# Kernel tuning notes

Measured on AMD Instinct MI355X. Metric: run time of the kernel, lower is better.

The kernel has to match this reference:

```python
import jax, jax.numpy as jnp
import numpy as np

B, T, C, H = 2, 2048, 1024, 16
D = C // H  # head dim = 64

def setup_inputs() -> dict:
    key = jax.random.key(0)
    ks = jax.random.split(key, 6)
    s = 0.02
    return {
        "x":  jax.random.normal(ks[0], (B, T, C), dtype=jnp.float32),
        "Wk": jax.random.normal(ks[1], (C, C), dtype=jnp.float32) * s,
        "Wq": jax.random.normal(ks[2], (C, C), dtype=jnp.float32) * s,
        "Wv": jax.random.normal(ks[3], (C, C), dtype=jnp.float32) * s,
        "Wp": jax.random.normal(ks[4], (C, C), dtype=jnp.float32) * s,
        "bp": jax.random.normal(ks[5], (C,), dtype=jnp.float32) * s,
    }

def reference(x, Wk, Wq, Wv, Wp, bp):
    Bs, Ts, Cs = x.shape
    # torch Linear: y = x @ W.T  (W is [out, in])
    def proj_heads(W):
        p = jnp.einsum('btc,dc->btd', x, W)
        return p.reshape(Bs, Ts, H, D).transpose(0, 2, 1, 3)  # [B,H,T,D]
    k = proj_heads(Wk)
    q = proj_heads(Wq)
    v = proj_heads(Wv)
    scale = 1.0 / jnp.sqrt(jnp.asarray(D, dtype=x.dtype))
    att = jnp.einsum('bhtd,bhsd->bhts', q, k) * scale  # [B,H,T,T]
    att = jax.nn.softmax(att, axis=-1)  # NOTE: no causal mask in the original forward
    y = jnp.einsum('bhts,bhsd->bhtd', att, v)
    y = y.transpose(0, 2, 1, 3).reshape(Bs, Ts, Cs)
    return jnp.einsum('btc,dc->btd', y, Wp) + bp
```

## Files before the change

### kernel.cpp

```cpp
#include <hip/hip_runtime.h>
#include <hip/hip_bf16.h>


typedef __bf16 bf16x8 __attribute__((ext_vector_type(8)));
typedef __bf16 bf16x4 __attribute__((ext_vector_type(4)));
typedef float  f32x4  __attribute__((ext_vector_type(4)));
typedef unsigned int uint2v __attribute__((ext_vector_type(2)));

#define QSCALE 0.18033688011112042f

__device__ __forceinline__ void gload_lds16(const void* g, void* l) {
  __builtin_amdgcn_global_load_lds((const __attribute__((address_space(1))) void*)g,
                                   (__attribute__((address_space(3))) void*)l, 16, 0, 0);
}
__device__ __forceinline__ unsigned int lds_off(const void* p) {
  return (unsigned int)(uintptr_t)(__attribute__((address_space(3))) const char*)p;
}
template<int IMM>
__device__ __forceinline__ uint2v tr_b64(unsigned int addr) {
  uint2v r;
  asm volatile("ds_read_b64_tr_b16 %0, %1 offset:%2" : "=v"(r) : "v"(addr), "i"(IMM));
  return r;
}

__global__ __launch_bounds__(256) void cvt_bf16(
    const float* __restrict__ x,  const float* __restrict__ wq, const float* __restrict__ wk,
    const float* __restrict__ wv, const float* __restrict__ wp,
    __bf16* __restrict__ xb,  __bf16* __restrict__ wqb, __bf16* __restrict__ wkb,
    __bf16* __restrict__ wvb, __bf16* __restrict__ wpb) {
  long long i = ((long long)blockIdx.x * 256 + threadIdx.x) * 4;
  const float* src; __bf16* dst; long long off;
  if      (i < 4194304LL) { src = x;  dst = xb;  off = i; }
  else if (i < 5242880LL) { src = wq; dst = wqb; off = i - 4194304LL; }
  else if (i < 6291456LL) { src = wk; dst = wkb; off = i - 5242880LL; }
  else if (i < 7340032LL) { src = wv; dst = wvb; off = i - 6291456LL; }
  else                    { src = wp; dst = wpb; off = i - 7340032LL; }
  float4 v = *(const float4*)(src + off);
  bf16x4 o;
  o[0] = (__bf16)v.x; o[1] = (__bf16)v.y; o[2] = (__bf16)v.z; o[3] = (__bf16)v.w;
  *(bf16x4*)(dst + off) = o;
}

template<int MFR>
__device__ __forceinline__ void gemm_core(
    const __bf16* __restrict__ A, const __bf16* __restrict__ Bw,
    int tileM, int tileN, char* smA, char* smB, f32x4 (&acc)[MFR][4]) {
  const int tid = threadIdx.x;
  const int lane = tid & 63;
  const int wid = tid >> 6;
  const int wr = wid >> 1, wc = wid & 1;
  #pragma unroll 1
  for (int k0 = 0; k0 < 1024; k0 += 64) {
    __syncthreads();
    #pragma unroll
    for (int r = 0; r < MFR; ++r) {
      int ci = tid + 256 * r;
      int row = ci >> 3, c = ci & 7;
      int sc = (c ^ (row & 7)) * 8;
      gload_lds16(A + (long long)(tileM + row) * 1024 + k0 + sc, smA + ci * 16);
    }
    #pragma unroll
    for (int r = 0; r < 4; ++r) {
      int ci = tid + 256 * r;
      int row = ci >> 3, c = ci & 7;
      int sc = (c ^ (row & 7)) * 8;
      gload_lds16(Bw + (long long)(tileN + row) * 1024 + k0 + sc, smB + ci * 16);
    }
    __syncthreads();
    #pragma unroll
    for (int kk = 0; kk < 2; ++kk) {
      bf16x8 af[MFR], bfr[4];
      #pragma unroll
      for (int i = 0; i < MFR; ++i) {
        int mrow = wr * (MFR * 16) + i * 16 + (lane & 15);
        af[i] = *(const bf16x8*)(smA + mrow * 128 +
                  ((kk * 64 + (lane >> 4) * 16) ^ ((mrow & 7) << 4)));
      }
      #pragma unroll
      for (int i = 0; i < 4; ++i) {
        int nrow = wc * 64 + i * 16 + (lane & 15);
        bfr[i] = *(const bf16x8*)(smB + nrow * 128 +
                  ((kk * 64 + (lane >> 4) * 16) ^ ((nrow & 7) << 4)));
      }
      __builtin_amdgcn_s_setprio(1);
      #pragma unroll
      for (int mi = 0; mi < MFR; ++mi)
        #pragma unroll
        for (int ni = 0; ni < 4; ++ni)
          acc[mi][ni] = __builtin_amdgcn_mfma_f32_16x16x32_bf16(af[mi], bfr[ni], acc[mi][ni], 0, 0, 0);
      __builtin_amdgcn_s_setprio(0);
    }
  }
}

__global__ __launch_bounds__(256) void gemm_qkv(
    const __bf16* __restrict__ Xb, const __bf16* __restrict__ Wqb,
    const __bf16* __restrict__ Wkb, const __bf16* __restrict__ Wvb,
    __bf16* __restrict__ Qh, __bf16* __restrict__ Kh, __bf16* __restrict__ Vh) {
  __shared__ __align__(16) char smA[16384];
  __shared__ __align__(16) char smB[16384];
  const int z = blockIdx.z;
  const __bf16* W = (z == 0) ? Wqb : (z == 1) ? Wkb : Wvb;
  __bf16* dst     = (z == 0) ? Qh  : (z == 1) ? Kh  : Vh;
  const float scale = (z == 0) ? QSCALE : 1.0f;
  const int tileM = blockIdx.x * 128, tileN = blockIdx.y * 128;
  f32x4 acc[4][4] = {};
  gemm_core<4>(Xb, W, tileM, tileN, smA, smB, acc);
  const int lane = threadIdx.x & 63, wid = threadIdx.x >> 6;
  const int wr = wid >> 1, wc = wid & 1;
  #pragma unroll
  for (int mi = 0; mi < 4; ++mi) {
    #pragma unroll
    for (int ni = 0; ni < 4; ++ni) {
      int n = tileN + wc * 64 + ni * 16 + (lane & 15);
      int h = n >> 6, d = n & 63;
      #pragma unroll
      for (int r = 0; r < 4; ++r) {
        int m = tileM + wr * 64 + mi * 16 + (lane >> 4) * 4 + r;
        int b = m >> 11, t = m & 2047;
        dst[((b * 16 + h) * 2048 + t) * 64 + d] = (__bf16)(acc[mi][ni][r] * scale);
      }
    }
  }
}

__global__ __launch_bounds__(256) void gemm_proj(
    const __bf16* __restrict__ Yb, const __bf16* __restrict__ Wpb,
    const float* __restrict__ bias, float* __restrict__ out) {
  __shared__ __align__(16) char smA[8192];
  __shared__ __align__(16) char smB[16384];
  const int tileM = blockIdx.x * 64, tileN = blockIdx.y * 128;
  f32x4 acc[2][4] = {};
  gemm_core<2>(Yb, Wpb, tileM, tileN, smA, smB, acc);
  const int lane = threadIdx.x & 63, wid = threadIdx.x >> 6;
  const int wr = wid >> 1, wc = wid & 1;
  #pragma unroll
  for (int mi = 0; mi < 2; ++mi) {
    #pragma unroll
    for (int ni = 0; ni < 4; ++ni) {
      int n = tileN + wc * 64 + ni * 16 + (lane & 15);
      float bv = bias[n];
      #pragma unroll
      for (int r = 0; r < 4; ++r) {
        int m = tileM + wr * 32 + mi * 16 + (lane >> 4) * 4 + r;
        out[(long long)m * 1024 + n] = acc[mi][ni][r] + bv;
      }
    }
  }
}

template<int KS>
__device__ __forceinline__ void pv_half(unsigned int trP, unsigned int trV,
                                        f32x4 Oa[2][4], f32x4 Osum[2], bf16x8 ones) {
  uint2v pl[2], ph[2];
  pl[0] = tr_b64<0 * 2048 + KS * 1024      >(trP);
  ph[0] = tr_b64<0 * 2048 + KS * 1024 + 512>(trP);
  pl[1] = tr_b64<1 * 2048 + KS * 1024      >(trP);
  ph[1] = tr_b64<1 * 2048 + KS * 1024 + 512>(trP);
  uint2v t0[4], t1[4];
  t0[0] = tr_b64<KS * 1024 + 0 * 2048>(trV);  t1[0] = tr_b64<KS * 1024 + 0 * 2048 + 512>(trV);
  t0[1] = tr_b64<KS * 1024 + 1 * 2048>(trV);  t1[1] = tr_b64<KS * 1024 + 1 * 2048 + 512>(trV);
  t0[2] = tr_b64<KS * 1024 + 2 * 2048>(trV);  t1[2] = tr_b64<KS * 1024 + 2 * 2048 + 512>(trV);
  t0[3] = tr_b64<KS * 1024 + 3 * 2048>(trV);  t1[3] = tr_b64<KS * 1024 + 3 * 2048 + 512>(trV);
  asm volatile("s_waitcnt lgkmcnt(0)");
  __builtin_amdgcn_sched_barrier(0);
  __builtin_amdgcn_s_setprio(1);
  bf16x8 pa[2];
  #pragma unroll
  for (int mi = 0; mi < 2; ++mi) {
    uint4 u; u.x = pl[mi][0]; u.y = pl[mi][1]; u.z = ph[mi][0]; u.w = ph[mi][1];
    pa[mi] = __builtin_bit_cast(bf16x8, u);
    Osum[mi] = __builtin_amdgcn_mfma_f32_16x16x32_bf16(pa[mi], ones, Osum[mi], 0, 0, 0);
  }
  #pragma unroll
  for (int nd = 0; nd < 4; ++nd) {
    uint4 u; u.x = t0[nd][0]; u.y = t0[nd][1]; u.z = t1[nd][0]; u.w = t1[nd][1];
    bf16x8 vf = __builtin_bit_cast(bf16x8, u);
    #pragma unroll
    for (int mi = 0; mi < 2; ++mi)
      Oa[mi][nd] = __builtin_amdgcn_mfma_f32_16x16x32_bf16(pa[mi], vf, Oa[mi][nd], 0, 0, 0);
  }
  __builtin_amdgcn_s_setprio(0);
}

__global__ __launch_bounds__(512, 4) void attn(
    const __bf16* __restrict__ Qh, const __bf16* __restrict__ Kh,
    const __bf16* __restrict__ Vh, float* __restrict__ Opart,
    float* __restrict__ lpart) {
  __shared__ __align__(16) char Ksm[2][8192];
  __shared__ __align__(16) char Vsm[2][8192];
  __shared__ __align__(16) char Psm[32768];
  const int tid = threadIdx.x, lane = tid & 63, wid = tid >> 6;
  const int lo = lane & 15, hi = lane >> 4;
  const int bh = blockIdx.x;
  const int qb = blockIdx.y;
  const int split = blockIdx.z;
  const int base = bh * (2048 * 64);
  const int qrow0 = qb * 256 + wid * 32;
  const int key0 = split * 1024;

  bf16x8 qf[2][2];
  #pragma unroll
  for (int mi = 0; mi < 2; ++mi)
    #pragma unroll
    for (int kk = 0; kk < 2; ++kk)
      qf[mi][kk] = *(const bf16x8*)(Qh + base + (qrow0 + mi * 16 + lo) * 64
                                    + kk * 32 + hi * 8);

  bf16x8 ones;
  #pragma unroll
  for (int j = 0; j < 8; ++j) ones[j] = (__bf16)1.0f;

  f32x4 Oa[2][4] = {};
  f32x4 Osum[2] = {};
  const unsigned int trP = lds_off(Psm) + wid * 4096 + lane * 8;

  unsigned int koff[4];
  #pragma unroll
  for (int ni = 0; ni < 4; ++ni) {
    int row = ni * 16 + lo;
    koff[ni] = row * 128 + ((hi * 16) ^ ((row & 7) << 4));
  }
  unsigned int paddr[2][4];
  #pragma unroll
  for (int mi = 0; mi < 2; ++mi)
    #pragma unroll
    for (int ni = 0; ni < 4; ++ni) {
      int kq = ni * 16 + lo;
      paddr[mi][ni] = wid * 4096 + mi * 2048 + (kq >> 5) * 1024 + ((kq >> 2) & 1) * 512 +
                      ((kq >> 3) & 3) * 128 + (kq & 3) * 32 + hi * 8;
    }

  int krow = tid >> 3, kc = tid & 7;
  int ksrc = base + (key0 + krow) * 64 + (kc ^ (krow & 7)) * 8;
  int kdst = tid * 16;
  int vcc = tid >> 6, vks = vcc & 1, vd4 = vcc >> 1;
  int vkey = vks * 32 + ((lane >> 3) & 3) * 8 + ((lane >> 5) & 1) * 4 + ((lane >> 1) & 3);
  int vsrc = base + (key0 + vkey) * 64 + vd4 * 16 + (lane & 1) * 8;
  int vdst = vks * 1024 + vd4 * 2048 + lane * 16;

  gload_lds16(Kh + ksrc, &Ksm[0][0] + kdst);
  gload_lds16(Vh + vsrc, &Vsm[0][0] + vdst);
  __syncthreads();
  int buf = 0;

  #pragma unroll 1
  for (int kt = 0; kt < 16; ++kt) {
    if (kt < 15) {
      gload_lds16(Kh + ksrc + (kt + 1) * 4096, &Ksm[buf ^ 1][0] + kdst);
      gload_lds16(Vh + vsrc + (kt + 1) * 4096, &Vsm[buf ^ 1][0] + vdst);
    }
    __builtin_amdgcn_sched_barrier(0);

    const char* Kb = &Ksm[buf][0];
    const unsigned int trV = lds_off(Vsm) + buf * 8192 + lane * 8;

    f32x4 S[2][4] = {};
    #pragma unroll
    for (int kk = 0; kk < 2; ++kk) {
      bf16x8 kf[4];
      #pragma unroll
      for (int ni = 0; ni < 4; ++ni)
        kf[ni] = *(const bf16x8*)(Kb + (koff[ni] ^ (kk * 64)));
      __builtin_amdgcn_s_setprio(1);
      #pragma unroll
      for (int mi = 0; mi < 2; ++mi)
        #pragma unroll
        for (int ni = 0; ni < 4; ++ni)
          S[mi][ni] = __builtin_amdgcn_mfma_f32_16x16x32_bf16(qf[mi][kk], kf[ni], S[mi][ni], 0, 0, 0);
      __builtin_amdgcn_s_setprio(0);
    }

    #pragma unroll
    for (int mi = 0; mi < 2; ++mi) {
      #pragma unroll
      for (int ni = 0; ni < 4; ++ni) {
        bf16x4 pb;
        #pragma unroll
        for (int r = 0; r < 4; ++r) pb[r] = (__bf16)exp2f(S[mi][ni][r]);
        *(bf16x4*)(&Psm[0] + paddr[mi][ni]) = pb;
      }
    }

    pv_half<0>(trP, trV, Oa, Osum, ones);
    pv_half<1>(trP, trV, Oa, Osum, ones);

    __syncthreads();
    buf ^= 1;
  }

  float* Op = Opart + (long long)(split * 32 + bh) * 2048 * 64;
  float* lp = lpart + (split * 32 + bh) * 2048;
  #pragma unroll
  for (int mi = 0; mi < 2; ++mi) {
    #pragma unroll
    for (int r = 0; r < 4; ++r) {
      int t = qrow0 + mi * 16 + hi * 4 + r;
      if (lo == 0) lp[t] = Osum[mi][r];
      #pragma unroll
      for (int nd = 0; nd < 4; ++nd)
        Op[(long long)t * 64 + nd * 16 + lo] = Oa[mi][nd][r];
    }
  }
}

__global__ __launch_bounds__(256) void attn_combine(
    const float* __restrict__ Opart, const float* __restrict__ lpart,
    __bf16* __restrict__ Yb) {
  int i = blockIdx.x * 256 + threadIdx.x;
  int row = i >> 4;
  int d0 = (i & 15) * 4;
  float4 o0 = *(const float4*)(Opart + (long long)row * 64 + d0);
  float4 o1 = *(const float4*)(Opart + 4194304LL + (long long)row * 64 + d0);
  float inv = 1.0f / (lpart[row] + lpart[65536 + row]);
  int bh = row >> 11, t = row & 2047;
  int b = bh >> 4, h = bh & 15;
  bf16x4 o;
  o[0] = (__bf16)((o0.x + o1.x) * inv); o[1] = (__bf16)((o0.y + o1.y) * inv);
  o[2] = (__bf16)((o0.z + o1.z) * inv); o[3] = (__bf16)((o0.w + o1.w) * inv);
  *(bf16x4*)(Yb + ((long long)(b * 2048 + t)) * 1024 + h * 64 + d0) = o;
}

extern "C" void kernel_launch(void* const* d_in, const int* in_sizes, int n_in,
                              void* d_out, int out_size, void* d_ws, size_t ws_size,
                              hipStream_t stream) {
  const float* x  = (const float*)d_in[0];
  const float* Wk = (const float*)d_in[1];
  const float* Wq = (const float*)d_in[2];
  const float* Wv = (const float*)d_in[3];
  const float* Wp = (const float*)d_in[4];
  const float* bp = (const float*)d_in[5];
  float* out = (float*)d_out;

  char* ws = (char*)d_ws;
  __bf16* Xb  = (__bf16*)ws;
  __bf16* Wqb = Xb  + 4194304;
  __bf16* Wkb = Wqb + 1048576;
  __bf16* Wvb = Wkb + 1048576;
  __bf16* Wpb = Wvb + 1048576;
  __bf16* Qh  = Wpb + 1048576;
  __bf16* Kh  = Qh  + 4194304;
  __bf16* Vh  = Kh  + 4194304;
  __bf16* Yb  = Vh  + 4194304;
  float*  Opart = (float*)(Yb + 4194304);
  float*  lpart = Opart + 8388608;

  cvt_bf16<<<8192, 256, 0, stream>>>(x, Wq, Wk, Wv, Wp, Xb, Wqb, Wkb, Wvb, Wpb);
  gemm_qkv<<<dim3(32, 8, 3), 256, 0, stream>>>(Xb, Wqb, Wkb, Wvb, Qh, Kh, Vh);
  attn<<<dim3(32, 8, 2), 512, 0, stream>>>(Qh, Kh, Vh, Opart, lpart);
  attn_combine<<<4096, 256, 0, stream>>>(Opart, lpart, Yb);
  gemm_proj<<<dim3(64, 8), 256, 0, stream>>>(Yb, Wpb, bp, out);
}
```

Measured before the change: 189.2 us.

## Double-buffer GEMM LDS tiles and merge QKV weights into one concatenated GEMM

The GEMM core now prefetches the next K-slice into a second LDS buffer with global_load_lds while MFMAs run on the current buffer, leaving one barrier per iteration instead of two. The QKV GEMM treats Wq/Wk/Wv as one contiguous 3072x1024 weight, since they sit back to back in the workspace, and uses a 2D grid. Q, K and V likewise sit back to back in the workspace, so each output goes to its slice with the Q scale kept. LDS use doubles (64KB for QKV), which may lower occupancy. The wait for the prefetched loads before reuse depends on the trailing barrier.

```diff
diff --git a/kernel.cpp b/kernel.cpp
--- a/kernel.cpp
+++ b/kernel.cpp
@@ -49,37 +49,58 @@
   const int lane = tid & 63;
   const int wid = tid >> 6;
   const int wr = wid >> 1, wc = wid & 1;
+  const int ABUF = MFR * 4096;
+
+  long long asrc[MFR]; int adst[MFR];
+  long long bsrc[4];   int bdst[4];
+  #pragma unroll
+  for (int r = 0; r < MFR; ++r) {
+    int ci = tid + 256 * r;
+    int row = ci >> 3, c = ci & 7;
+    asrc[r] = (long long)(tileM + row) * 1024 + (c ^ (row & 7)) * 8;
+    adst[r] = ci * 16;
+  }
+  #pragma unroll
+  for (int r = 0; r < 4; ++r) {
+    int ci = tid + 256 * r;
+    int row = ci >> 3, c = ci & 7;
+    bsrc[r] = (long long)(tileN + row) * 1024 + (c ^ (row & 7)) * 8;
+    bdst[r] = ci * 16;
+  }
+
+  #pragma unroll
+  for (int r = 0; r < MFR; ++r) gload_lds16(A + asrc[r], smA + adst[r]);
+  #pragma unroll
+  for (int r = 0; r < 4; ++r)   gload_lds16(Bw + bsrc[r], smB + bdst[r]);
+  __syncthreads();
+  int buf = 0;
+
   #pragma unroll 1
   for (int k0 = 0; k0 < 1024; k0 += 64) {
-    __syncthreads();
-    #pragma unroll
-    for (int r = 0; r < MFR; ++r) {
-      int ci = tid + 256 * r;
-      int row = ci >> 3, c = ci & 7;
-      int sc = (c ^ (row & 7)) * 8;
-      gload_lds16(A + (long long)(tileM + row) * 1024 + k0 + sc, smA + ci * 16);
-    }
-    #pragma unroll
-    for (int r = 0; r < 4; ++r) {
-      int ci = tid + 256 * r;
-      int row = ci >> 3, c = ci & 7;
-      int sc = (c ^ (row & 7)) * 8;
-      gload_lds16(Bw + (long long)(tileN + row) * 1024 + k0 + sc, smB + ci * 16);
-    }
-    __syncthreads();
+    if (k0 + 64 < 1024) {
+      #pragma unroll
+      for (int r = 0; r < MFR; ++r)
+        gload_lds16(A + asrc[r] + k0 + 64, smA + (buf ^ 1) * ABUF + adst[r]);
+      #pragma unroll
+      for (int r = 0; r < 4; ++r)
+        gload_lds16(Bw + bsrc[r] + k0 + 64, smB + (buf ^ 1) * 16384 + bdst[r]);
+    }
+    __builtin_amdgcn_sched_barrier(0);
+    const char* sA = smA + buf * ABUF;
+    const char* sB = smB + buf * 16384;
     #pragma unroll
     for (int kk = 0; kk < 2; ++kk) {
       bf16x8 af[MFR], bfr[4];
       #pragma unroll
       for (int i = 0; i < MFR; ++i) {
         int mrow = wr * (MFR * 16) + i * 16 + (lane & 15);
-        af[i] = *(const bf16x8*)(smA + mrow * 128 +
+        af[i] = *(const bf16x8*)(sA + mrow * 128 +
                   ((kk * 64 + (lane >> 4) * 16) ^ ((mrow & 7) << 4)));
       }
       #pragma unroll
       for (int i = 0; i < 4; ++i) {
         int nrow = wc * 64 + i * 16 + (lane & 15);
-        bfr[i] = *(const bf16x8*)(smB + nrow * 128 +
+        bfr[i] = *(const bf16x8*)(sB + nrow * 128 +
                   ((kk * 64 + (lane >> 4) * 16) ^ ((nrow & 7) << 4)));
       }
       __builtin_amdgcn_s_setprio(1);
@@ -90,29 +111,29 @@
           acc[mi][ni] = __builtin_amdgcn_mfma_f32_16x16x32_bf16(af[mi], bfr[ni], acc[mi][ni], 0, 0, 0);
       __builtin_amdgcn_s_setprio(0);
     }
+    __syncthreads();
+    buf ^= 1;
   }
 }
 
 __global__ __launch_bounds__(256) void gemm_qkv(
-    const __bf16* __restrict__ Xb, const __bf16* __restrict__ Wqb,
-    const __bf16* __restrict__ Wkb, const __bf16* __restrict__ Wvb,
-    __bf16* __restrict__ Qh, __bf16* __restrict__ Kh, __bf16* __restrict__ Vh) {
-  __shared__ __align__(16) char smA[16384];
-  __shared__ __align__(16) char smB[16384];
-  const int z = blockIdx.z;
-  const __bf16* W = (z == 0) ? Wqb : (z == 1) ? Wkb : Wvb;
-  __bf16* dst     = (z == 0) ? Qh  : (z == 1) ? Kh  : Vh;
-  const float scale = (z == 0) ? QSCALE : 1.0f;
+    const __bf16* __restrict__ Xb, const __bf16* __restrict__ Wcat,
+    __bf16* __restrict__ QKVh) {
+  __shared__ __align__(16) char smA[32768];
+  __shared__ __align__(16) char smB[32768];
   const int tileM = blockIdx.x * 128, tileN = blockIdx.y * 128;
   f32x4 acc[4][4] = {};
-  gemm_core<4>(Xb, W, tileM, tileN, smA, smB, acc);
+  gemm_core<4>(Xb, Wcat, tileM, tileN, smA, smB, acc);
+  const int z = tileN >> 10;
+  const float scale = (z == 0) ? QSCALE : 1.0f;
+  __bf16* dst = QKVh + (long long)z * 4194304;
   const int lane = threadIdx.x & 63, wid = threadIdx.x >> 6;
   const int wr = wid >> 1, wc = wid & 1;
   #pragma unroll
   for (int mi = 0; mi < 4; ++mi) {
     #pragma unroll
     for (int ni = 0; ni < 4; ++ni) {
-      int n = tileN + wc * 64 + ni * 16 + (lane & 15);
+      int n = (tileN & 1023) + wc * 64 + ni * 16 + (lane & 15);
       int h = n >> 6, d = n & 63;
       #pragma unroll
       for (int r = 0; r < 4; ++r) {
@@ -127,8 +148,8 @@
 __global__ __launch_bounds__(256) void gemm_proj(
     const __bf16* __restrict__ Yb, const __bf16* __restrict__ Wpb,
     const float* __restrict__ bias, float* __restrict__ out) {
-  __shared__ __align__(16) char smA[8192];
-  __shared__ __align__(16) char smB[16384];
+  __shared__ __align__(16) char smA[16384];
+  __shared__ __align__(16) char smB[32768];
   const int tileM = blockIdx.x * 64, tileN = blockIdx.y * 128;
   f32x4 acc[2][4] = {};
   gemm_core<2>(Yb, Wpb, tileM, tileN, smA, smB, acc);
@@ -346,7 +367,7 @@
   float*  lpart = Opart + 8388608;
 
   cvt_bf16<<<8192, 256, 0, stream>>>(x, Wq, Wk, Wv, Wp, Xb, Wqb, Wkb, Wvb, Wpb);
-  gemm_qkv<<<dim3(32, 8, 3), 256, 0, stream>>>(Xb, Wqb, Wkb, Wvb, Qh, Kh, Vh);
+  gemm_qkv<<<dim3(32, 24), 256, 0, stream>>>(Xb, Wqb, Qh);
   attn<<<dim3(32, 8, 2), 512, 0, stream>>>(Qh, Kh, Vh, Opart, lpart);
   attn_combine<<<4096, 256, 0, stream>>>(Opart, lpart, Yb);
   gemm_proj<<<dim3(64, 8), 256, 0, stream>>>(Yb, Wpb, bp, out);
```

Measured after the change: 200.3 us. +5.8%, slower.

## Rewrite QKV GEMM as 256x256 double-buffered tile kernel over concatenated weights

Applied to the files above, without the earlier changes.

Replaces the 128x128 single-buffered QKV projection with a 512-thread 256x256-tile kernel. It treats Wq/Wk/Wv as one contiguous concatenated weight matrix, which works because they sit back to back in the workspace, and likewise writes Q/K/V as one contiguous output. Global-to-LDS loads for the next K step are double-buffered and interleaved between MFMA phases, gated by explicit vmcnt waits and raw barriers. The aim is more data reuse per tile and overlap of memory transfer with compute, at the cost of 128KB of LDS and heavy register pressure. With only 192 blocks, wave quantization becomes a risk.

```diff
diff --git a/kernel.cpp b/kernel.cpp
--- a/kernel.cpp
+++ b/kernel.cpp
@@ -41,8 +41,126 @@
   *(bf16x4*)(dst + off) = o;
 }
 
+__device__ __forceinline__ void stage_half(const __bf16* src, int s0, int s1,
+                                           char* d, int d0, int d1) {
+  gload_lds16(src + s0, d + d0);
+  gload_lds16(src + s1, d + d1);
+}
+
+template<int Q, int KK, bool LB>
+__device__ __forceinline__ void qkv_phase(const char* pA, const char* pB,
+    const unsigned int (&aoff)[2], bf16x8 (&bfr)[4], f32x4 (&acc)[8][4]) {
+  bf16x8 af[4];
+  #pragma unroll
+  for (int i = 0; i < 4; ++i)
+    af[i] = *(const bf16x8*)(pA + (Q * 4 + i) * 2048 + aoff[KK]);
+  if constexpr (LB) {
+    #pragma unroll
+    for (int n = 0; n < 4; ++n)
+      bfr[n] = *(const bf16x8*)(pB + n * 2048 + aoff[KK]);
+  }
+  __builtin_amdgcn_s_setprio(1);
+  #pragma unroll
+  for (int mi = 0; mi < 4; ++mi)
+    #pragma unroll
+    for (int n = 0; n < 4; ++n)
+      acc[Q * 4 + mi][n] =
+        __builtin_amdgcn_mfma_f32_16x16x32_bf16(af[mi], bfr[n], acc[Q * 4 + mi][n], 0, 0, 0);
+  __builtin_amdgcn_s_setprio(0);
+}
+
+__global__ __launch_bounds__(512, 2) void gemm_qkv(
+    const __bf16* __restrict__ Xb, const __bf16* __restrict__ Wcat,
+    __bf16* __restrict__ QKVh) {
+  __shared__ __align__(16) char smA[2][2][16384];
+  __shared__ __align__(16) char smB[2][2][16384];
+  const int tid = threadIdx.x, lane = tid & 63, wid = tid >> 6;
+  const int lo = lane & 15, hi = lane >> 4;
+  const int wr = wid >> 2, wc = wid & 3;
+  const int tileM = blockIdx.x * 256, tileN = blockIdx.y * 256;
+
+  int asrc[2][2], bsrc[2][2], sdst[2];
+  #pragma unroll
+  for (int r = 0; r < 2; ++r) {
+    int ci = r * 512 + tid;
+    int row = ci >> 3, c = ci & 7;
+    int sc = (c ^ (row & 7)) * 8;
+    sdst[r] = ci * 16;
+    #pragma unroll
+    for (int h = 0; h < 2; ++h) {
+      asrc[h][r] = (tileM + h * 128 + row) * 1024 + sc;
+      bsrc[h][r] = (tileN + h * 128 + row) * 1024 + sc;
+    }
+  }
+  unsigned int aoff[2];
+  aoff[0] = lo * 128 + ((hi * 16) ^ ((lo & 7) << 4));
+  aoff[1] = lo * 128 + ((64 + hi * 16) ^ ((lo & 7) << 4));
+
+  f32x4 acc[8][4] = {};
+
+  stage_half(Xb,   asrc[0][0], asrc[0][1], &smA[0][0][0], sdst[0], sdst[1]);
+  stage_half(Wcat, bsrc[0][0], bsrc[0][1], &smB[0][0][0], sdst[0], sdst[1]);
+  stage_half(Wcat, bsrc[1][0], bsrc[1][1], &smB[0][1][0], sdst[0], sdst[1]);
+  stage_half(Xb,   asrc[1][0], asrc[1][1], &smA[0][1][0], sdst[0], sdst[1]);
+
+  int buf = 0;
+  #pragma unroll 1
+  for (int t = 0; t < 16; ++t) {
+    const char* pA = &smA[buf][wr][0];
+    const char* pB = &smB[buf][wc >> 1][0] + (wc & 1) * 8192;
+    char* nA0 = &smA[buf ^ 1][0][0];
+    char* nA1 = &smA[buf ^ 1][1][0];
+    char* nB0 = &smB[buf ^ 1][0][0];
+    char* nB1 = &smB[buf ^ 1][1][0];
+    const int ko = (t + 1) * 64;
+    bf16x8 bfr[4];
+    if (t < 15) {
+      stage_half(Xb, asrc[0][0] + ko, asrc[0][1] + ko, nA0, sdst[0], sdst[1]);
+      asm volatile("s_waitcnt vmcnt(2)" ::: "memory");
+    } else {
+      asm volatile("s_waitcnt vmcnt(0)" ::: "memory");
+    }
+    __builtin_amdgcn_s_barrier();
+    asm volatile("" ::: "memory");
+    qkv_phase<0, 0, true >(pA, pB, aoff, bfr, acc);
+    if (t < 15) {
+      stage_half(Wcat, bsrc[0][0] + ko, bsrc[0][1] + ko, nB0, sdst[0], sdst[1]);
+      stage_half(Wcat, bsrc[1][0] + ko, bsrc[1][1] + ko, nB1, sdst[0], sdst[1]);
+    }
+    qkv_phase<1, 0, false>(pA, pB, aoff, bfr, acc);
+    if (t < 15) {
+      stage_half(Xb, asrc[1][0] + ko, asrc[1][1] + ko, nA1, sdst[0], sdst[1]);
+    }
+    qkv_phase<0, 1, true >(pA, pB, aoff, bfr, acc);
+    qkv_phase<1, 1, false>(pA, pB, aoff, bfr, acc);
+    asm volatile("" ::: "memory");
+    __builtin_amdgcn_s_barrier();
+    asm volatile("" ::: "memory");
+    buf ^= 1;
+  }
+
+  const int z = tileN >> 10;
+  const float scale = (z == 0) ? QSCALE : 1.0f;
+  __bf16* dst = QKVh + (long long)z * 4194304;
+  const int nbase = (tileN & 1023) + wc * 64;
+  #pragma unroll
+  for (int m = 0; m < 8; ++m) {
+    #pragma unroll
+    for (int n = 0; n < 4; ++n) {
+      int ncol = nbase + n * 16 + lo;
+      int h = ncol >> 6, d = ncol & 63;
+      #pragma unroll
+      for (int r = 0; r < 4; ++r) {
+        int mg = tileM + wr * 128 + m * 16 + hi * 4 + r;
+        int b = mg >> 11, tt = mg & 2047;
+        dst[((b * 16 + h) * 2048 + tt) * 64 + d] = (__bf16)(acc[m][n][r] * scale);
+      }
+    }
+  }
+}
+
 template<int MFR>
-__device__ __forceinline__ void gemm_core(
+__device__ __forceinline__ void gemm_core_sb(
     const __bf16* __restrict__ A, const __bf16* __restrict__ Bw,
     int tileM, int tileN, char* smA, char* smB, f32x4 (&acc)[MFR][4]) {
   const int tid = threadIdx.x;
@@ -93,37 +211,6 @@
   }
 }
 
-__global__ __launch_bounds__(256) void gemm_qkv(
-    const __bf16* __restrict__ Xb, const __bf16* __restrict__ Wqb,
-    const __bf16* __restrict__ Wkb, const __bf16* __restrict__ Wvb,
-    __bf16* __restrict__ Qh, __bf16* __restrict__ Kh, __bf16* __restrict__ Vh) {
-  __shared__ __align__(16) char smA[16384];
-  __shared__ __align__(16) char smB[16384];
-  const int z = blockIdx.z;
-  const __bf16* W = (z == 0) ? Wqb : (z == 1) ? Wkb : Wvb;
-  __bf16* dst     = (z == 0) ? Qh  : (z == 1) ? Kh  : Vh;
-  const float scale = (z == 0) ? QSCALE : 1.0f;
-  const int tileM = blockIdx.x * 128, tileN = blockIdx.y * 128;
-  f32x4 acc[4][4] = {};
-  gemm_core<4>(Xb, W, tileM, tileN, smA, smB, acc);
-  const int lane = threadIdx.x & 63, wid = threadIdx.x >> 6;
-  const int wr = wid >> 1, wc = wid & 1;
-  #pragma unroll
-  for (int mi = 0; mi < 4; ++mi) {
-    #pragma unroll
-    for (int ni = 0; ni < 4; ++ni) {
-      int n = tileN + wc * 64 + ni * 16 + (lane & 15);
-      int h = n >> 6, d = n & 63;
-      #pragma unroll
-      for (int r = 0; r < 4; ++r) {
-        int m = tileM + wr * 64 + mi * 16 + (lane >> 4) * 4 + r;
-        int b = m >> 11, t = m & 2047;
-        dst[((b * 16 + h) * 2048 + t) * 64 + d] = (__bf16)(acc[mi][ni][r] * scale);
-      }
-    }
-  }
-}
-
 __global__ __launch_bounds__(256) void gemm_proj(
     const __bf16* __restrict__ Yb, const __bf16* __restrict__ Wpb,
     const float* __restrict__ bias, float* __restrict__ out) {
@@ -131,7 +218,7 @@
   __shared__ __align__(16) char smB[16384];
   const int tileM = blockIdx.x * 64, tileN = blockIdx.y * 128;
   f32x4 acc[2][4] = {};
-  gemm_core<2>(Yb, Wpb, tileM, tileN, smA, smB, acc);
+  gemm_core_sb<2>(Yb, Wpb, tileM, tileN, smA, smB, acc);
   const int lane = threadIdx.x & 63, wid = threadIdx.x >> 6;
   const int wr = wid >> 1, wc = wid & 1;
   #pragma unroll
@@ -346,7 +433,7 @@
   float*  lpart = Opart + 8388608;
 
   cvt_bf16<<<8192, 256, 0, stream>>>(x, Wq, Wk, Wv, Wp, Xb, Wqb, Wkb, Wvb, Wpb);
-  gemm_qkv<<<dim3(32, 8, 3), 256, 0, stream>>>(Xb, Wqb, Wkb, Wvb, Qh, Kh, Vh);
+  gemm_qkv<<<dim3(16, 12), 512, 0, stream>>>(Xb, Wqb, Qh);
   attn<<<dim3(32, 8, 2), 512, 0, stream>>>(Qh, Kh, Vh, Opart, lpart);
   attn_combine<<<4096, 256, 0, stream>>>(Opart, lpart, Yb);
   gemm_proj<<<dim3(64, 8), 256, 0, stream>>>(Yb, Wpb, bp, out);
```

Measured after the change: 201.1 us. 6.3% more time.

## Fuse split-attention combine into output projection GEMM A-tile load

Applied to the files above, without the earlier changes.

Removes the separate attn_combine kernel. The projection GEMM now reads the two fp32 partial outputs and row sums directly, normalizes them, packs them to bf16 and writes the A tile into LDS. The softmax exponent stores also switch to packed v_cvt_pk_bf16_f32 conversions. This drops one launch and the round trip of Yb through memory, but each of the 8 N-tile blocks rereads the fp32 partials, which raises global traffic, and A loads become synchronous register loads instead of direct-to-LDS loads.

```diff
diff --git a/kernel.cpp b/kernel.cpp
--- a/kernel.cpp
+++ b/kernel.cpp
@@ -20,6 +20,11 @@
 __device__ __forceinline__ uint2v tr_b64(unsigned int addr) {
   uint2v r;
   asm volatile("ds_read_b64_tr_b16 %0, %1 offset:%2" : "=v"(r) : "v"(addr), "i"(IMM));
+  return r;
+}
+__device__ __forceinline__ unsigned int cvtpk_bf16(float a, float b) {
+  unsigned int r;
+  asm("v_cvt_pk_bf16_f32 %0, %1, %2" : "=v"(r) : "v"(a), "v"(b));
   return r;
 }
 
@@ -42,7 +47,7 @@
 }
 
 template<int MFR>
-__device__ __forceinline__ void gemm_core(
+__device__ __forceinline__ void gemm_core_sb(
     const __bf16* __restrict__ A, const __bf16* __restrict__ Bw,
     int tileM, int tileN, char* smA, char* smB, f32x4 (&acc)[MFR][4]) {
   const int tid = threadIdx.x;
@@ -105,7 +110,7 @@
   const float scale = (z == 0) ? QSCALE : 1.0f;
   const int tileM = blockIdx.x * 128, tileN = blockIdx.y * 128;
   f32x4 acc[4][4] = {};
-  gemm_core<4>(Xb, W, tileM, tileN, smA, smB, acc);
+  gemm_core_sb<4>(Xb, W, tileM, tileN, smA, smB, acc);
   const int lane = threadIdx.x & 63, wid = threadIdx.x >> 6;
   const int wr = wid >> 1, wc = wid & 1;
   #pragma unroll
@@ -125,15 +130,86 @@
 }
 
 __global__ __launch_bounds__(256) void gemm_proj(
-    const __bf16* __restrict__ Yb, const __bf16* __restrict__ Wpb,
-    const float* __restrict__ bias, float* __restrict__ out) {
+    const float* __restrict__ Opart, const float* __restrict__ lpart,
+    const __bf16* __restrict__ Wpb, const float* __restrict__ bias,
+    float* __restrict__ out) {
   __shared__ __align__(16) char smA[8192];
   __shared__ __align__(16) char smB[16384];
+  const int tid = threadIdx.x, lane = tid & 63, wid = tid >> 6;
+  const int wr = wid >> 1, wc = wid & 1;
   const int tileM = blockIdx.x * 64, tileN = blockIdx.y * 128;
   f32x4 acc[2][4] = {};
-  gemm_core<2>(Yb, Wpb, tileM, tileN, smA, smB, acc);
-  const int lane = threadIdx.x & 63, wid = threadIdx.x >> 6;
-  const int wr = wid >> 1, wc = wid & 1;
+
+  int aoff0[2], al0[2], adst[2];
+  #pragma unroll
+  for (int r = 0; r < 2; ++r) {
+    int ci = tid + 256 * r;
+    int row = ci >> 3, c = ci & 7;
+    int d0 = (c ^ (row & 7)) * 8;
+    int m = tileM + row;
+    int b = m >> 11, t = m & 2047;
+    aoff0[r] = b * 2097152 + t * 64 + d0;
+    al0[r]   = b * 32768 + t;
+    adst[r]  = ci * 16;
+  }
+  long long bsrc[4]; int bdst[4];
+  #pragma unroll
+  for (int r = 0; r < 4; ++r) {
+    int ci = tid + 256 * r;
+    int row = ci >> 3, c = ci & 7;
+    bsrc[r] = (long long)(tileN + row) * 1024 + (c ^ (row & 7)) * 8;
+    bdst[r] = ci * 16;
+  }
+
+  #pragma unroll 1
+  for (int ks = 0; ks < 16; ++ks) {
+    __syncthreads();
+    #pragma unroll
+    for (int r = 0; r < 4; ++r)
+      gload_lds16(Wpb + bsrc[r] + ks * 64, smB + bdst[r]);
+    #pragma unroll
+    for (int r = 0; r < 2; ++r) {
+      const float* p0 = Opart + aoff0[r] + ks * 131072;
+      const float* p1 = p0 + 4194304;
+      float4 x0 = *(const float4*)p0;
+      float4 x1 = *(const float4*)(p0 + 4);
+      float4 y0 = *(const float4*)p1;
+      float4 y1 = *(const float4*)(p1 + 4);
+      int li = al0[r] + ks * 2048;
+      float inv = 1.0f / (lpart[li] + lpart[65536 + li]);
+      uint4 w;
+      w.x = cvtpk_bf16((x0.x + y0.x) * inv, (x0.y + y0.y) * inv);
+      w.y = cvtpk_bf16((x0.z + y0.z) * inv, (x0.w + y0.w) * inv);
+      w.z = cvtpk_bf16((x1.x + y1.x) * inv, (x1.y + y1.y) * inv);
+      w.w = cvtpk_bf16((x1.z + y1.z) * inv, (x1.w + y1.w) * inv);
+      *(uint4*)(smA + adst[r]) = w;
+    }
+    __syncthreads();
+    #pragma unroll
+    for (int kk = 0; kk < 2; ++kk) {
+      bf16x8 af[2], bfr[4];
+      #pragma unroll
+      for (int i = 0; i < 2; ++i) {
+        int mrow = wr * 32 + i * 16 + (lane & 15);
+        af[i] = *(const bf16x8*)(smA + mrow * 128 +
+                  ((kk * 64 + (lane >> 4) * 16) ^ ((mrow & 7) << 4)));
+      }
+      #pragma unroll
+      for (int i = 0; i < 4; ++i) {
+        int nrow = wc * 64 + i * 16 + (lane & 15);
+        bfr[i] = *(const bf16x8*)(smB + nrow * 128 +
+                  ((kk * 64 + (lane >> 4) * 16) ^ ((nrow & 7) << 4)));
+      }
+      __builtin_amdgcn_s_setprio(1);
+      #pragma unroll
+      for (int mi = 0; mi < 2; ++mi)
+        #pragma unroll
+        for (int ni = 0; ni < 4; ++ni)
+          acc[mi][ni] = __builtin_amdgcn_mfma_f32_16x16x32_bf16(af[mi], bfr[ni], acc[mi][ni], 0, 0, 0);
+      __builtin_amdgcn_s_setprio(0);
+    }
+  }
+
   #pragma unroll
   for (int mi = 0; mi < 2; ++mi) {
     #pragma unroll
@@ -275,10 +351,14 @@
     for (int mi = 0; mi < 2; ++mi) {
       #pragma unroll
       for (int ni = 0; ni < 4; ++ni) {
-        bf16x4 pb;
-        #pragma unroll
-        for (int r = 0; r < 4; ++r) pb[r] = (__bf16)exp2f(S[mi][ni][r]);
-        *(bf16x4*)(&Psm[0] + paddr[mi][ni]) = pb;
+        float e0 = exp2f(S[mi][ni][0]);
+        float e1 = exp2f(S[mi][ni][1]);
+        float e2 = exp2f(S[mi][ni][2]);
+        float e3 = exp2f(S[mi][ni][3]);
+        uint2v w;
+        w[0] = cvtpk_bf16(e0, e1);
+        w[1] = cvtpk_bf16(e2, e3);
+        *(uint2v*)(&Psm[0] + paddr[mi][ni]) = w;
       }
     }
 
@@ -302,23 +382,6 @@
         Op[(long long)t * 64 + nd * 16 + lo] = Oa[mi][nd][r];
     }
   }
-}
-
-__global__ __launch_bounds__(256) void attn_combine(
-    const float* __restrict__ Opart, const float* __restrict__ lpart,
-    __bf16* __restrict__ Yb) {
-  int i = blockIdx.x * 256 + threadIdx.x;
-  int row = i >> 4;
-  int d0 = (i & 15) * 4;
-  float4 o0 = *(const float4*)(Opart + (long long)row * 64 + d0);
-  float4 o1 = *(const float4*)(Opart + 4194304LL + (long long)row * 64 + d0);
-  float inv = 1.0f / (lpart[row] + lpart[65536 + row]);
-  int bh = row >> 11, t = row & 2047;
-  int b = bh >> 4, h = bh & 15;
-  bf16x4 o;
-  o[0] = (__bf16)((o0.x + o1.x) * inv); o[1] = (__bf16)((o0.y + o1.y) * inv);
-  o[2] = (__bf16)((o0.z + o1.z) * inv); o[3] = (__bf16)((o0.w + o1.w) * inv);
-  *(bf16x4*)(Yb + ((long long)(b * 2048 + t)) * 1024 + h * 64 + d0) = o;
 }
 
 extern "C" void kernel_launch(void* const* d_in, const int* in_sizes, int n_in,
@@ -348,6 +411,5 @@
   cvt_bf16<<<8192, 256, 0, stream>>>(x, Wq, Wk, Wv, Wp, Xb, Wqb, Wkb, Wvb, Wpb);
   gemm_qkv<<<dim3(32, 8, 3), 256, 0, stream>>>(Xb, Wqb, Wkb, Wvb, Qh, Kh, Vh);
   attn<<<dim3(32, 8, 2), 512, 0, stream>>>(Qh, Kh, Vh, Opart, lpart);
-  attn_combine<<<4096, 256, 0, stream>>>(Opart, lpart, Yb);
-  gemm_proj<<<dim3(64, 8), 256, 0, stream>>>(Yb, Wpb, bp, out);
-}
+  gemm_proj<<<dim3(64, 8), 256, 0, stream>>>(Opart, lpart, Wpb, bp, out);
+}
```

Measured after the change: 190.6 us. No clear change (+0.7%).
